# Kernel tuning notes

Hardware: AMD Instinct MI355X
Metric: run time of the kernel (lower is better)

The kernel has to match this reference:

```python
import jax, jax.numpy as jnp
import numpy as np


def conv1x1(x, w, b):
    # x: [B,C,H,W], w: [O,C], b: [O] -> [B,O,H,W]
    return jnp.einsum('bchw,oc->bohw', x, w) + b[None, :, None, None]


def setup_inputs() -> dict:
    key = jax.random.key(0)
    ks = jax.random.split(key, 8)
    B, C, H, W = 16, 256, 64, 64
    Cq = C // 8
    x = jax.random.normal(ks[0], (B, C, H, W), dtype=jnp.float32)
    wq = jax.random.normal(ks[1], (Cq, C), dtype=jnp.float32) * (2.0 / C) ** 0.5
    bq = jnp.zeros((Cq,), dtype=jnp.float32)
    wk = jax.random.normal(ks[2], (Cq, C), dtype=jnp.float32) * (2.0 / C) ** 0.5
    bk = jnp.zeros((Cq,), dtype=jnp.float32)
    wv = jax.random.normal(ks[3], (C, C), dtype=jnp.float32) * (2.0 / C) ** 0.5
    bv = jnp.zeros((C,), dtype=jnp.float32)
    gamma = jax.random.normal(ks[4], (1,), dtype=jnp.float32) * 0.1
    return {'x': x, 'wq': wq, 'bq': bq, 'wk': wk, 'bk': bk, 'wv': wv, 'bv': bv, 'gamma': gamma}


def reference(x, wq, bq, wk, bk, wv, bv, gamma):
    B, C, H, W = x.shape
    bH = B // 4
    bW = B // 4  # requires bH*bW == B, i.e. B == 16
    q = conv1x1(x, wq, bq)   # [B, C/8, H, W]
    k = conv1x1(x, wk, bk)   # [B, C/8, H, W]
    v = conv1x1(x, wv, bv)   # [B, C, H, W]
    # batch index b -> grid (h = b // bW, w = b % bW); token feature = flat map
    qg = q.reshape(bH, bW, -1)  # [bH, bW, Dq]
    kg = k.reshape(bH, bW, -1)
    vg = v.reshape(bH, bW, -1)  # [bH, bW, Dv]
    # column ('H') attention with -inf diagonal, row ('W') attention
    eH = jnp.einsum('hwd,gwd->hwg', qg, kg)  # [bH, bW, bH]
    eye = jnp.eye(bH, dtype=bool)[:, None, :]  # mask h == h'
    eH = jnp.where(eye, -jnp.inf, eH)
    eW = jnp.einsum('hwd,hgd->hwg', qg, kg)  # [bH, bW, bW]
    att = jax.nn.softmax(jnp.concatenate([eH, eW], axis=-1), axis=-1)
    aH, aW = att[..., :bH], att[..., bH:]
    oH = jnp.einsum('hwg,gwd->hwd', aH, vg)  # attend down the column
    oW = jnp.einsum('hwg,hgd->hwd', aW, vg)  # attend along the row
    out = (oH + oW).reshape(B, C, H, W)
    return gamma[0] * out + x
```

## Files before the change

kernel.cpp:

```cpp
#include <hip/hip_runtime.h>

#define B_   16
#define C_   256
#define HW_  4096
#define DQK  131072
#define DV   1048576

using bf16x8  = __attribute__((ext_vector_type(8))) __bf16;
using ushort8 = __attribute__((ext_vector_type(8))) unsigned short;
using u16x4   = __attribute__((ext_vector_type(4))) unsigned short;
using f32x4   = __attribute__((ext_vector_type(4))) float;

static __device__ __forceinline__ unsigned short f2bf(float f) {
    union { float f; unsigned u; } v; v.f = f;
    unsigned r = v.u + 0x7FFFu + ((v.u >> 16) & 1u);
    return (unsigned short)(r >> 16);
}
static __device__ __forceinline__ float bf2f(unsigned short h) {
    union { unsigned u; float f; } v; v.u = ((unsigned)h) << 16;
    return v.f;
}

__global__ __launch_bounds__(256) void k_pack(const float* wq, const float* wk, const float* wv,
                                              unsigned short* Wh, unsigned short* Wl, unsigned short* Wv) {
    int idx = blockIdx.x * 256 + threadIdx.x;
    if (idx < 16384) {
        float f = (idx < 8192) ? wq[idx] : wk[idx - 8192];
        unsigned short hi = f2bf(f);
        Wh[idx] = hi;
        Wl[idx] = f2bf(f - bf2f(hi));
    } else {
        int i = idx - 16384;
        Wv[i] = f2bf(wv[i]);
    }
}

__global__ __launch_bounds__(256) void k_gemm_qk(const unsigned short* __restrict__ Wh,
                                                 const unsigned short* __restrict__ Wl,
                                                 const float* __restrict__ x,
                                                 const float* __restrict__ bq, const float* __restrict__ bk,
                                                 float* __restrict__ QF, float* __restrict__ KF) {
    __shared__ __align__(16) unsigned short Ah[64][40], Al[64][40];
    __shared__ __align__(16) unsigned short Bh[128][40], Bl[128][40];
    int b  = blockIdx.y;
    int n0 = blockIdx.x * 128;
    int t = threadIdx.x;
    int lane = t & 63, wid = t >> 6;
    int wm = wid >> 1, wn = wid & 1;
    int lr = lane & 15, kg = lane >> 4;

    const float* xb = x + (size_t)b * DV;
    int am = t >> 2, akq = (t & 3) * 8;
    int bkr = t >> 3, bnq = (t & 7) * 16;
    int swz_w = (t & 3) << 3;
    int colw  = bkr ^ swz_w;

    f32x4 acc[2][4];
    for (int mi = 0; mi < 2; mi++)
        for (int ni = 0; ni < 4; ni++) acc[mi][ni] = (f32x4){0.f, 0.f, 0.f, 0.f};

    for (int kk = 0; kk < 8; kk++) {
        int k0 = kk * 32;
        *(ushort8*)&Ah[am][akq] = *(const ushort8*)(Wh + (size_t)am * 256 + k0 + akq);
        *(ushort8*)&Al[am][akq] = *(const ushort8*)(Wl + (size_t)am * 256 + k0 + akq);
        const float* srcb = xb + (size_t)(k0 + bkr) * HW_ + n0 + bnq;
        for (int e4 = 0; e4 < 4; e4++) {
            f32x4 v = *(const f32x4*)(srcb + e4 * 4);
            for (int e = 0; e < 4; e++) {
                float f = v[e];
                unsigned short hi = f2bf(f);
                int row = bnq + e4 * 4 + e;
                Bh[row][colw] = hi;
                Bl[row][colw] = f2bf(f - bf2f(hi));
            }
        }
        __syncthreads();
        bf16x8 ah[2], al[2], bh[4], bl[4];
        for (int mi = 0; mi < 2; mi++) {
            ah[mi] = *(const bf16x8*)&Ah[wm * 32 + mi * 16 + lr][kg * 8];
            al[mi] = *(const bf16x8*)&Al[wm * 32 + mi * 16 + lr][kg * 8];
        }
        for (int ni = 0; ni < 4; ni++) {
            int row = wn * 64 + ni * 16 + lr;
            int cg  = (kg ^ ((wn * 4 + ni) & 3)) * 8;
            bh[ni] = *(const bf16x8*)&Bh[row][cg];
            bl[ni] = *(const bf16x8*)&Bl[row][cg];
        }
        for (int mi = 0; mi < 2; mi++)
            for (int ni = 0; ni < 4; ni++) {
                acc[mi][ni] = __builtin_amdgcn_mfma_f32_16x16x32_bf16(ah[mi], bh[ni], acc[mi][ni], 0, 0, 0);
                acc[mi][ni] = __builtin_amdgcn_mfma_f32_16x16x32_bf16(ah[mi], bl[ni], acc[mi][ni], 0, 0, 0);
                acc[mi][ni] = __builtin_amdgcn_mfma_f32_16x16x32_bf16(al[mi], bh[ni], acc[mi][ni], 0, 0, 0);
            }
        __syncthreads();
    }
    for (int mi = 0; mi < 2; mi++) {
        int mbase = wm * 32 + mi * 16 + kg * 4;
        for (int i = 0; i < 4; i++) {
            int m = mbase + i;
            float bias = (m < 32) ? bq[m] : bk[m - 32];
            for (int ni = 0; ni < 4; ni++) {
                int n = n0 + wn * 64 + ni * 16 + lr;
                float val = acc[mi][ni][i] + bias;
                if (m < 32) QF[(size_t)b * DQK + (size_t)m * HW_ + n] = val;
                else        KF[(size_t)b * DQK + (size_t)(m - 32) * HW_ + n] = val;
            }
        }
    }
}

__global__ __launch_bounds__(256) void k_scores2(const float* __restrict__ QF, const float* __restrict__ KF,
                                                 float* __restrict__ Sp) {
    __shared__ float Ql[16][520], Kl[16][520];
    int s = blockIdx.x;
    int m = s >> 3, off = (s & 7) * 512;
    int t = threadIdx.x;
    for (int b = 0; b < 16; b++) {
        const float* qs = QF + (size_t)b * DQK + (size_t)m * HW_ + off;
        const float* ks = KF + (size_t)b * DQK + (size_t)m * HW_ + off;
        Ql[b][t]       = qs[t];
        Ql[b][t + 256] = qs[t + 256];
        Kl[b][t]       = ks[t];
        Kl[b][t + 256] = ks[t + 256];
    }
    __syncthreads();
    int p = t >> 1, h = t & 1;
    int b = p >> 3, j = p & 7;
    int hb = b >> 2, wb = b & 3;
    int bp = (j < 4) ? (j * 4 + wb) : (hb * 4 + (j - 4));
    const f32x4* q4 = (const f32x4*)&Ql[b][h * 256];
    const f32x4* k4 = (const f32x4*)&Kl[bp][h * 256];
    f32x4 a4 = (f32x4){0.f, 0.f, 0.f, 0.f};
    for (int i = 0; i < 64; i++) a4 += q4[i] * k4[i];
    float sres = a4[0] + a4[1] + a4[2] + a4[3];
    sres += __shfl_xor(sres, 1);
    if (h == 0) Sp[(size_t)p * 256 + s] = sres;
}

__global__ void k_softmax2(const float* __restrict__ Sp, const float* __restrict__ gamma,
                           float* __restrict__ Mm) {
    __shared__ float SS[128];
    int t = threadIdx.x;
    const f32x4* s4 = (const f32x4*)(Sp + (size_t)t * 256);
    f32x4 a = (f32x4){0.f, 0.f, 0.f, 0.f};
    for (int i = 0; i < 64; i++) a += s4[i];
    SS[t] = a[0] + a[1] + a[2] + a[3];
    __syncthreads();
    if (t < 16) {
        int b = t, h = b >> 2, w = b & 3;
        float e[8];
        for (int j = 0; j < 8; j++) e[j] = SS[b * 8 + j];
        e[h] = -INFINITY;
        float mx = e[0];
        for (int j = 1; j < 8; j++) mx = fmaxf(mx, e[j]);
        float aa[8], sum = 0.f;
        for (int j = 0; j < 8; j++) { aa[j] = expf(e[j] - mx); sum += aa[j]; }
        float inv = 1.0f / sum;
        float g = gamma[0];
        float row[16];
        for (int c = 0; c < 16; c++) row[c] = 0.f;
        for (int gg = 0; gg < 4; gg++) if (gg != h) row[gg * 4 + w] += aa[gg] * inv;
        for (int gg = 0; gg < 4; gg++) row[h * 4 + gg] += aa[4 + gg] * inv;
        for (int c = 0; c < 16; c++) Mm[b * 16 + c] = row[c] * g;
        Mm[256 + b] = g;
    }
}

__global__ __launch_bounds__(256) void k_mix(const float* __restrict__ Mm, const float* __restrict__ x,
                                             unsigned short* __restrict__ Xm) {
    __shared__ float Ms[256];
    __shared__ unsigned short T[16][32][36];
    int t = threadIdx.x;
    int p0 = blockIdx.x * 32, cb = blockIdx.y, c0 = cb * 32;
    Ms[t] = Mm[t];

    int c_l = t >> 3, p4 = t & 7;
    f32x4 in4[16];
    for (int bp = 0; bp < 16; bp++)
        in4[bp] = *(const f32x4*)(x + (size_t)bp * DV + (size_t)(c0 + c_l) * HW_ + p0 + p4 * 4);
    __syncthreads();
    for (int b = 0; b < 16; b++) {
        f32x4 acc = (f32x4){0.f, 0.f, 0.f, 0.f};
        for (int bp = 0; bp < 16; bp++) {
            float wgt = Ms[b * 16 + bp];
            acc += wgt * in4[bp];
        }
        for (int e = 0; e < 4; e++) T[b][p4 * 4 + e][c_l] = f2bf(acc[e]);
    }
    __syncthreads();
    int p_l = t >> 3, cq = t & 7;
    for (int b = 0; b < 16; b++) {
        u16x4 v = *(const u16x4*)&T[b][p_l][cq * 4];
        *(u16x4*)(Xm + ((size_t)(b * 8 + cb) * HW_ + p0 + p_l) * 32 + cq * 4) = v;
    }
}

__global__ __launch_bounds__(256) void k_gemm_v_res(const unsigned short* __restrict__ Wv,
                                                    const unsigned short* __restrict__ Xm,
                                                    const float* __restrict__ bv,
                                                    const float* __restrict__ MmRs,
                                                    const float* __restrict__ x,
                                                    float* __restrict__ out) {
    __shared__ __align__(16) unsigned short As[64][72];
    __shared__ __align__(16) unsigned short Bs[128][72];
    int b  = blockIdx.z;
    int m0 = blockIdx.y * 64;
    int n0 = blockIdx.x * 128;
    int t = threadIdx.x;
    int lane = t & 63, wid = t >> 6;
    int wm = wid >> 1, wn = wid & 1;
    int lr = lane & 15, kg = lane >> 4;

    int am = t >> 2, aq = (t & 3) * 16;
    int bn = t >> 1, half = t & 1;

    f32x4 acc[2][4];
    for (int mi = 0; mi < 2; mi++)
        for (int ni = 0; ni < 4; ni++) acc[mi][ni] = (f32x4){0.f, 0.f, 0.f, 0.f};

    for (int kk = 0; kk < 4; kk++) {
        int k0 = kk * 64;
        *(ushort8*)&As[am][aq]     = *(const ushort8*)(Wv + (size_t)(m0 + am) * 256 + k0 + aq);
        *(ushort8*)&As[am][aq + 8] = *(const ushort8*)(Wv + (size_t)(m0 + am) * 256 + k0 + aq + 8);
        const unsigned short* c0p = Xm + ((size_t)(b * 8 + kk * 2)     * HW_ + n0 + bn) * 32 + half * 16;
        const unsigned short* c1p = Xm + ((size_t)(b * 8 + kk * 2 + 1) * HW_ + n0 + bn) * 32 + half * 16;
        *(ushort8*)&Bs[bn][half * 16]          = *(const ushort8*)(c0p);
        *(ushort8*)&Bs[bn][half * 16 + 8]      = *(const ushort8*)(c0p + 8);
        *(ushort8*)&Bs[bn][32 + half * 16]     = *(const ushort8*)(c1p);
        *(ushort8*)&Bs[bn][32 + half * 16 + 8] = *(const ushort8*)(c1p + 8);
        __syncthreads();
        for (int ks = 0; ks < 2; ks++) {
            bf16x8 a[2], bb[4];
            for (int mi = 0; mi < 2; mi++) a[mi]  = *(const bf16x8*)&As[wm * 32 + mi * 16 + lr][ks * 32 + kg * 8];
            for (int ni = 0; ni < 4; ni++) bb[ni] = *(const bf16x8*)&Bs[wn * 64 + ni * 16 + lr][ks * 32 + kg * 8];
            for (int mi = 0; mi < 2; mi++)
                for (int ni = 0; ni < 4; ni++)
                    acc[mi][ni] = __builtin_amdgcn_mfma_f32_16x16x32_bf16(a[mi], bb[ni], acc[mi][ni], 0, 0, 0);
        }
        __syncthreads();
    }
    float rs_b = MmRs[256 + b];
    for (int mi = 0; mi < 2; mi++) {
        int mbase = m0 + wm * 32 + mi * 16 + kg * 4;
        for (int i = 0; i < 4; i++) {
            int m = mbase + i;
            float bias = rs_b * bv[m];
            for (int ni = 0; ni < 4; ni++) {
                int n = n0 + wn * 64 + ni * 16 + lr;
                size_t idx = (size_t)b * DV + (size_t)m * HW_ + n;
                out[idx] = acc[mi][ni][i] + bias + x[idx];
            }
        }
    }
}

extern "C" void kernel_launch(void* const* d_in, const int* in_sizes, int n_in,
                              void* d_out, int out_size, void* d_ws, size_t ws_size,
                              hipStream_t stream) {
    (void)in_sizes; (void)n_in; (void)out_size; (void)ws_size;
    const float* x     = (const float*)d_in[0];
    const float* wq    = (const float*)d_in[1];
    const float* bq    = (const float*)d_in[2];
    const float* wk    = (const float*)d_in[3];
    const float* bk    = (const float*)d_in[4];
    const float* wv    = (const float*)d_in[5];
    const float* bv    = (const float*)d_in[6];
    const float* gamma = (const float*)d_in[7];

    char* ws = (char*)d_ws;
    unsigned short* Wh = (unsigned short*)(ws + 0);
    unsigned short* Wl = (unsigned short*)(ws + 32768);
    unsigned short* Wv = (unsigned short*)(ws + 65536);
    float*          QF = (float*)(ws + 196608);
    float*          KF = (float*)(ws + 8585216);
    unsigned short* Xm = (unsigned short*)(ws + 16973824);
    float*          Sp = (float*)(ws + 16973824);
    float*          Mm = (float*)(ws + 0);
    float*          vo = (float*)d_out;

    k_pack       <<<320, 256, 0, stream>>>(wq, wk, wv, Wh, Wl, Wv);
    k_gemm_qk    <<<dim3(32, 16), 256, 0, stream>>>(Wh, Wl, x, bq, bk, QF, KF);
    k_scores2    <<<256, 256, 0, stream>>>(QF, KF, Sp);
    k_softmax2   <<<1, 128, 0, stream>>>(Sp, gamma, Mm);
    k_mix        <<<dim3(128, 8), 256, 0, stream>>>(Mm, x, Xm);
    k_gemm_v_res <<<dim3(32, 4, 16), 256, 0, stream>>>(Wv, Xm, bv, Mm, x, vo);
}
```

Before: 99.79 us.

## Pre-tile Wv and mixed activations into MFMA fragment layout, drop LDS staging

Wv is packed and the mixed bf16 activations are written in a 16-row-by-8-column fragment-tiled layout, so each lane can load its MFMA operand straight from global memory with one contiguous 16-byte read. The V-GEMM no longer stages through shared memory and has no barriers. The block tile changes to 128x64, with each wave covering 64x32. This removes LDS traffic and synchronisation but depends on L2/cache reuse for operands that were previously shared across a block through LDS.

```diff
diff --git a/kernel.cpp b/kernel.cpp
--- a/kernel.cpp
+++ b/kernel.cpp
@@ -31,7 +31,9 @@
         Wl[idx] = f2bf(f - bf2f(hi));
     } else {
         int i = idx - 16384;
-        Wv[i] = f2bf(wv[i]);
+        int mt = i >> 12, kt = (i >> 7) & 31, lr = (i >> 3) & 15, j = i & 7;
+        int m = mt * 16 + lr, c = kt * 8 + j;
+        Wv[i] = f2bf(wv[m * 256 + c]);
     }
 }
 
@@ -171,7 +173,7 @@
     __shared__ float Ms[256];
     __shared__ unsigned short T[16][32][36];
     int t = threadIdx.x;
-    int p0 = blockIdx.x * 32, cb = blockIdx.y, c0 = cb * 32;
+    int p0 = blockIdx.x * 32, c0 = blockIdx.y * 32;
     Ms[t] = Mm[t];
 
     int c_l = t >> 3, p4 = t & 7;
@@ -189,66 +191,56 @@
     }
     __syncthreads();
     int p_l = t >> 3, cq = t & 7;
+    int p = p0 + p_l;
+    int c = c0 + cq * 4;
+    size_t dst = (size_t)(p >> 4) * 4096 + (size_t)(c >> 3) * 128 + (p & 15) * 8 + (c & 7);
     for (int b = 0; b < 16; b++) {
         u16x4 v = *(const u16x4*)&T[b][p_l][cq * 4];
-        *(u16x4*)(Xm + ((size_t)(b * 8 + cb) * HW_ + p0 + p_l) * 32 + cq * 4) = v;
-    }
-}
-
-__global__ __launch_bounds__(256) void k_gemm_v_res(const unsigned short* __restrict__ Wv,
-                                                    const unsigned short* __restrict__ Xm,
+        *(u16x4*)(Xm + (size_t)b * DV + dst) = v;
+    }
+}
+
+__global__ __launch_bounds__(256) void k_gemm_v_res(const unsigned short* __restrict__ Wvf,
+                                                    const unsigned short* __restrict__ Xmf,
                                                     const float* __restrict__ bv,
                                                     const float* __restrict__ MmRs,
                                                     const float* __restrict__ x,
                                                     float* __restrict__ out) {
-    __shared__ __align__(16) unsigned short As[64][72];
-    __shared__ __align__(16) unsigned short Bs[128][72];
     int b  = blockIdx.z;
-    int m0 = blockIdx.y * 64;
-    int n0 = blockIdx.x * 128;
+    int m0 = blockIdx.y * 128;
+    int n0 = blockIdx.x * 64;
     int t = threadIdx.x;
     int lane = t & 63, wid = t >> 6;
     int wm = wid >> 1, wn = wid & 1;
     int lr = lane & 15, kg = lane >> 4;
 
-    int am = t >> 2, aq = (t & 3) * 16;
-    int bn = t >> 1, half = t & 1;
-
-    f32x4 acc[2][4];
-    for (int mi = 0; mi < 2; mi++)
-        for (int ni = 0; ni < 4; ni++) acc[mi][ni] = (f32x4){0.f, 0.f, 0.f, 0.f};
-
-    for (int kk = 0; kk < 4; kk++) {
-        int k0 = kk * 64;
-        *(ushort8*)&As[am][aq]     = *(const ushort8*)(Wv + (size_t)(m0 + am) * 256 + k0 + aq);
-        *(ushort8*)&As[am][aq + 8] = *(const ushort8*)(Wv + (size_t)(m0 + am) * 256 + k0 + aq + 8);
-        const unsigned short* c0p = Xm + ((size_t)(b * 8 + kk * 2)     * HW_ + n0 + bn) * 32 + half * 16;
-        const unsigned short* c1p = Xm + ((size_t)(b * 8 + kk * 2 + 1) * HW_ + n0 + bn) * 32 + half * 16;
-        *(ushort8*)&Bs[bn][half * 16]          = *(const ushort8*)(c0p);
-        *(ushort8*)&Bs[bn][half * 16 + 8]      = *(const ushort8*)(c0p + 8);
-        *(ushort8*)&Bs[bn][32 + half * 16]     = *(const ushort8*)(c1p);
-        *(ushort8*)&Bs[bn][32 + half * 16 + 8] = *(const ushort8*)(c1p + 8);
-        __syncthreads();
-        for (int ks = 0; ks < 2; ks++) {
-            bf16x8 a[2], bb[4];
-            for (int mi = 0; mi < 2; mi++) a[mi]  = *(const bf16x8*)&As[wm * 32 + mi * 16 + lr][ks * 32 + kg * 8];
-            for (int ni = 0; ni < 4; ni++) bb[ni] = *(const bf16x8*)&Bs[wn * 64 + ni * 16 + lr][ks * 32 + kg * 8];
-            for (int mi = 0; mi < 2; mi++)
-                for (int ni = 0; ni < 4; ni++)
-                    acc[mi][ni] = __builtin_amdgcn_mfma_f32_16x16x32_bf16(a[mi], bb[ni], acc[mi][ni], 0, 0, 0);
-        }
-        __syncthreads();
-    }
+    const unsigned short* Ab = Wvf + (size_t)((m0 >> 4) + wm * 4) * 4096 + lane * 8;
+    const unsigned short* Bb = Xmf + (size_t)b * DV + (size_t)((n0 >> 4) + wn * 2) * 4096 + lane * 8;
+
+    f32x4 acc[4][2];
+    for (int mi = 0; mi < 4; mi++)
+        for (int ni = 0; ni < 2; ni++) acc[mi][ni] = (f32x4){0.f, 0.f, 0.f, 0.f};
+
+    #pragma unroll 4
+    for (int kk = 0; kk < 8; kk++) {
+        bf16x8 a[4], bb[2];
+        for (int mi = 0; mi < 4; mi++) a[mi]  = *(const bf16x8*)(Ab + (size_t)mi * 4096 + kk * 512);
+        for (int ni = 0; ni < 2; ni++) bb[ni] = *(const bf16x8*)(Bb + (size_t)ni * 4096 + kk * 512);
+        for (int mi = 0; mi < 4; mi++)
+            for (int ni = 0; ni < 2; ni++)
+                acc[mi][ni] = __builtin_amdgcn_mfma_f32_16x16x32_bf16(a[mi], bb[ni], acc[mi][ni], 0, 0, 0);
+    }
+
     float rs_b = MmRs[256 + b];
-    for (int mi = 0; mi < 2; mi++) {
-        int mbase = m0 + wm * 32 + mi * 16 + kg * 4;
+    for (int mi = 0; mi < 4; mi++) {
+        int mbase = m0 + wm * 64 + mi * 16 + kg * 4;
         for (int i = 0; i < 4; i++) {
             int m = mbase + i;
             float bias = rs_b * bv[m];
-            for (int ni = 0; ni < 4; ni++) {
-                int n = n0 + wn * 64 + ni * 16 + lr;
-                size_t idx = (size_t)b * DV + (size_t)m * HW_ + n;
-                out[idx] = acc[mi][ni][i] + bias + x[idx];
+            size_t rowoff = (size_t)b * DV + (size_t)m * HW_;
+            for (int ni = 0; ni < 2; ni++) {
+                int n = n0 + wn * 32 + ni * 16 + lr;
+                out[rowoff + n] = acc[mi][ni][i] + bias + x[rowoff + n];
             }
         }
     }
@@ -283,5 +275,5 @@
     k_scores2    <<<256, 256, 0, stream>>>(QF, KF, Sp);
     k_softmax2   <<<1, 128, 0, stream>>>(Sp, gamma, Mm);
     k_mix        <<<dim3(128, 8), 256, 0, stream>>>(Mm, x, Xm);
-    k_gemm_v_res <<<dim3(32, 4, 16), 256, 0, stream>>>(Wv, Xm, bv, Mm, x, vo);
-}
+    k_gemm_v_res <<<dim3(64, 2, 16), 256, 0, stream>>>(Wv, Xm, bv, Mm, x, vo);
+}
```

Result: faster. 92.39 us (-7.4%).
